# Performance work log

Measured on AMD Instinct MI355X. Metric: run time of the kernel, lower is better.

## Reference

```python
import jax, jax.numpy as jnp
import numpy as np

N = 50000   # team_count (num nodes)
E = 800000  # num edges
D = 64      # embed_dim
C = 32      # conv_out_channels
K = 3       # Chebyshev order
B = 16384   # number of games (len(home))


def setup_inputs() -> dict:
    key = jax.random.key(0)
    ks = jax.random.split(key, 20)
    inp = {
        "edge_index": jax.random.randint(ks[0], (2, E), 0, N),
        "home": jax.random.randint(ks[1], (B,), 0, N),
        "away": jax.random.randint(ks[2], (B,), 0, N),
        "edge_weight": jax.random.uniform(ks[3], (E,), dtype=jnp.float32),
        "embedding": jax.random.normal(ks[4], (N, D), dtype=jnp.float32) * 0.1,
    }
    def W(k, i, o):
        return jax.random.normal(k, (K, i, o), dtype=jnp.float32) * 0.05
    inp["Wxz"] = W(ks[5], D, C); inp["Whz"] = W(ks[6], C, C)
    inp["Wxr"] = W(ks[7], D, C); inp["Whr"] = W(ks[8], C, C)
    inp["Wxh"] = W(ks[9], D, C); inp["Whh"] = W(ks[10], C, C)
    for i, name in enumerate(["bxz", "bhz", "bxr", "bhr", "bxh", "bhh"]):
        inp[name] = jax.random.normal(ks[11 + i], (C,), dtype=jnp.float32) * 0.01
    return inp


def _cheb(x, W, b, row, col, w_hat, n):
    """PyG ChebConv with sym normalization, lambda_max=2: L_hat = -D^-1/2 A D^-1/2."""
    def prop(t):  # L_hat @ t  via gather->scale->scatter over edges
        return jax.ops.segment_sum(w_hat[:, None] * t[row], col, num_segments=n)
    Tx0 = x
    out = Tx0 @ W[0]
    Tx1 = prop(Tx0)
    out = out + Tx1 @ W[1]
    for k in range(2, W.shape[0]):
        Tx2 = 2.0 * prop(Tx1) - Tx0
        out = out + Tx2 @ W[k]
        Tx0, Tx1 = Tx1, Tx2
    return out + b


def reference(edge_index, home, away, edge_weight, embedding,
              Wxz, Whz, Wxr, Whr, Wxh, Whh,
              bxz, bhz, bxr, bhr, bxh, bhh):
    row, col = edge_index[0], edge_index[1]
    n = embedding.shape[0]
    deg = jax.ops.segment_sum(edge_weight, row, num_segments=n)
    dinv = jnp.where(deg > 0, jax.lax.rsqrt(deg), 0.0)
    w_hat = -dinv[row] * edge_weight * dinv[col]

    x = embedding                       # [N, D]
    H = jnp.zeros((n, Wxz.shape[-1]), x.dtype)  # initial hidden state
    cheb = lambda t, W, b: _cheb(t, W, b, row, col, w_hat, n)

    Z = jax.nn.sigmoid(cheb(x, Wxz, bxz) + cheb(H, Whz, bhz))
    R = jax.nn.sigmoid(cheb(x, Wxr, bxr) + cheb(H, Whr, bhr))
    H_tilde = jnp.tanh(cheb(x, Wxh, bxh) + cheb(H * R, Whh, bhh))
    H = Z * H + (1.0 - Z) * H_tilde     # [N, C]

    h = jnp.concatenate([H[home], H[away]], axis=0)  # [2B, C]
    return jax.nn.softmax(h, axis=0)    # torch Softmax(dim=0)
```

## Files before the change

kernel.cpp:

```cpp
#include <hip/hip_runtime.h>
#include <hip/hip_fp16.h>
#include <math.h>

constexpr int N_   = 50000;
constexpr int E_   = 800000;
constexpr int D_   = 64;
constexpr int C_   = 32;
constexpr int B_   = 16384;
constexpr int TWOB = 2 * B_;
constexpr int NB_SM = 256;
constexpr int NBINS = (N_ + 255) / 256;
constexpr int EPB   = 4096;
constexpr int NBLK_BIN = (E_ + EPB - 1) / EPB;
constexpr int CAPB  = 5120;
constexpr int GN  = 64;
constexpr int LDP = 68;
constexpr int NPAD = 50176;

__device__ inline float4 ld_h4(const ushort* p) {
    uint2 u = *reinterpret_cast<const uint2*>(p);
    __half2 h0 = *reinterpret_cast<__half2*>(&u.x);
    __half2 h1 = *reinterpret_cast<__half2*>(&u.y);
    float2 f0 = __half22float2(h0), f1 = __half22float2(h1);
    return make_float4(f0.x, f0.y, f1.x, f1.y);
}
__device__ inline void st_h4(ushort* p, float4 v) {
    __half2 h0 = __floats2half2_rn(v.x, v.y);
    __half2 h1 = __floats2half2_rn(v.z, v.w);
    uint2 u;
    u.x = *reinterpret_cast<unsigned*>(&h0);
    u.y = *reinterpret_cast<unsigned*>(&h1);
    *reinterpret_cast<uint2*>(p) = u;
}

__global__ __launch_bounds__(256) void k_init(const float* __restrict__ x,
                                              ushort* __restrict__ xh,
                                              int2* __restrict__ curs) {
    if (blockIdx.x == 0) {
        curs[threadIdx.x] = make_int2(0, 0);
        if (threadIdx.x < 32) curs[256 + threadIdx.x] = make_int2(0, 0);
    }
    int i = blockIdx.x * 256 + threadIdx.x;
    if (i < N_ * D_ / 4) {
        float4 v = reinterpret_cast<const float4*>(x)[i];
        st_h4(xh + (size_t)i * 4, v);
    }
}

__device__ inline void excl_scan256(int* sc, int t, int c0, int* st) {
    sc[t] = c0;
    __syncthreads();
#pragma unroll
    for (int off = 1; off < 256; off <<= 1) {
        int v = (t >= off) ? sc[t - off] : 0;
        __syncthreads();
        sc[t] += v;
        __syncthreads();
    }
    st[t] = sc[t] - c0;
}

__global__ __launch_bounds__(256) void k_bin(const int* __restrict__ row,
                                             const int* __restrict__ col,
                                             const float* __restrict__ ew,
                                             int* __restrict__ colCur,
                                             int* __restrict__ rowCur,
                                             int2* __restrict__ colBins,
                                             int2* __restrict__ rowBins) {
    __shared__ int cnt[256], st[256], cur[256], gbase[256], sc[256];
    __shared__ int2 buf[EPB];
    int t = threadIdx.x;
    int base = blockIdx.x * EPB;
    int nE = min(EPB, E_ - base);

    cnt[t] = 0;
    __syncthreads();
    for (int i = t; i < nE; i += 256) atomicAdd(&cnt[col[base + i] >> 8], 1);
    __syncthreads();
    int c0 = cnt[t];
    excl_scan256(sc, t, c0, st);
    cur[t] = 0;
    gbase[t] = (t < NBINS && c0 > 0) ? atomicAdd(&colCur[t], c0) : 0;
    __syncthreads();
    for (int i = t; i < nE; i += 256) {
        int c = col[base + i], r = row[base + i];
        float w = ew[base + i];
        int p = st[c >> 8] + atomicAdd(&cur[c >> 8], 1);
        buf[p] = make_int2((c << 16) | r, __float_as_int(w));
    }
    __syncthreads();
    for (int i = t; i < nE; i += 256) {
        int2 e = buf[i];
        int bin = (int)(((unsigned)e.x) >> 24);
        int local = gbase[bin] + (i - st[bin]);
        if (local < CAPB) colBins[(size_t)bin * CAPB + local] = e;
    }
    __syncthreads();

    cnt[t] = 0;
    __syncthreads();
    for (int i = t; i < nE; i += 256) atomicAdd(&cnt[row[base + i] >> 8], 1);
    __syncthreads();
    c0 = cnt[t];
    excl_scan256(sc, t, c0, st);
    cur[t] = 0;
    gbase[t] = (t < NBINS && c0 > 0) ? atomicAdd(&rowCur[t], c0) : 0;
    __syncthreads();
    for (int i = t; i < nE; i += 256) {
        int r = row[base + i];
        float w = ew[base + i];
        int p = st[r >> 8] + atomicAdd(&cur[r >> 8], 1);
        buf[p] = make_int2(r, __float_as_int(w));
    }
    __syncthreads();
    for (int i = t; i < nE; i += 256) {
        int2 e = buf[i];
        int bin = (int)(((unsigned)e.x) >> 8);
        int local = gbase[bin] + (i - st[bin]);
        if (local < CAPB) rowBins[(size_t)bin * CAPB + local] = e;
    }
}

__global__ __launch_bounds__(256) void k_deg(const int* __restrict__ rowCur,
                                             const int2* __restrict__ rowBins,
                                             float* __restrict__ dinv) {
    __shared__ float acc[256];
    int t = threadIdx.x, b = blockIdx.x;
    acc[t] = 0.f;
    __syncthreads();
    int nb = min(rowCur[b], CAPB);
    const int2* bb = rowBins + (size_t)b * CAPB;
    for (int i = t; i < nb; i += 256) {
        int2 e = bb[i];
        atomicAdd(&acc[e.x & 255], __int_as_float(e.y));
    }
    __syncthreads();
    int r = b * 256 + t;
    if (r < N_) {
        float d = acc[t];
        dinv[r] = (d > 0.f) ? 1.f / sqrtf(d) : 0.f;
    }
}

__global__ __launch_bounds__(256) void k_sort(const int* __restrict__ colCur,
                                              int2* __restrict__ colBins,
                                              const float* __restrict__ dinv,
                                              int2* __restrict__ percol) {
    __shared__ int cnt[256], st[256], cur[256], sc[256];
    __shared__ int2 sbuf[CAPB];
    int t = threadIdx.x, b = blockIdx.x;
    int nb = min(colCur[b], CAPB);
    int2* bb = colBins + (size_t)b * CAPB;
    cnt[t] = 0;
    __syncthreads();
    for (int i = t; i < nb; i += 256)
        atomicAdd(&cnt[(((unsigned)bb[i].x) >> 16) & 255], 1);
    __syncthreads();
    int c0 = cnt[t];
    excl_scan256(sc, t, c0, st);
    cur[t] = 0;
    __syncthreads();
    for (int i = t; i < nb; i += 256) {
        int2 e = bb[i];
        int clow = (((unsigned)e.x) >> 16) & 255;
        int p = st[clow] + atomicAdd(&cur[clow], 1);
        sbuf[p] = e;
    }
    __syncthreads();
    for (int i = t; i < nb; i += 256) {
        int2 e = sbuf[i];
        unsigned m = (unsigned)e.x;
        int r = (int)(m & 0xffffu);
        int c = (int)(m >> 16);
        float w = -__int_as_float(e.y) * dinv[r] * dinv[c];
        bb[i] = make_int2(r, __float_as_int(w));
    }
    int c = b * 256 + t;
    percol[c] = make_int2(b * CAPB + st[t], cnt[t]);
}

template <bool FUSE2>
__global__ __launch_bounds__(256) void k_gproph(const int2* __restrict__ percol,
                                                const int2* __restrict__ edges,
                                                const ushort* __restrict__ src,
                                                const ushort* __restrict__ xsub,
                                                ushort* __restrict__ dst) {
    int node = (blockIdx.x * 256 + threadIdx.x) >> 6;
    if (node >= N_) return;
    int lane = threadIdx.x & 63;
    int eslot = lane >> 4;
    int f4 = (lane & 15) << 2;
    int2 oc = percol[node];
    int beg = oc.x, n = oc.y;
    float4 acc = {0.f, 0.f, 0.f, 0.f};
    for (int cb = 0; cb < n; cb += 16) {
        int2 er = edges[beg + cb + (lane & 15)];
        int   rr = er.x;
        float wr = __int_as_float(er.y);
#pragma unroll
        for (int k = 0; k < 4; ++k) {
            int idx = cb + 4 * k + eslot;
            int   r = __shfl(rr, 4 * k + eslot, 64);
            float w = __shfl(wr, 4 * k + eslot, 64);
            bool ok = idx < n;
            int  rs = ok ? r : 0;
            float wm = ok ? w : 0.f;
            float4 v = ld_h4(src + (size_t)rs * D_ + f4);
            acc.x += wm * v.x;
            acc.y += wm * v.y;
            acc.z += wm * v.z;
            acc.w += wm * v.w;
        }
    }
    acc.x += __shfl_xor(acc.x, 16, 64); acc.y += __shfl_xor(acc.y, 16, 64);
    acc.z += __shfl_xor(acc.z, 16, 64); acc.w += __shfl_xor(acc.w, 16, 64);
    acc.x += __shfl_xor(acc.x, 32, 64); acc.y += __shfl_xor(acc.y, 32, 64);
    acc.z += __shfl_xor(acc.z, 32, 64); acc.w += __shfl_xor(acc.w, 32, 64);
    if (eslot == 0) {
        float4 o = acc;
        if (FUSE2) {
            float4 xv = ld_h4(xsub + (size_t)node * D_ + f4);
            o.x = 2.f * acc.x - xv.x;
            o.y = 2.f * acc.y - xv.y;
            o.z = 2.f * acc.z - xv.z;
            o.w = 2.f * acc.w - xv.w;
        }
        st_h4(dst + (size_t)node * D_ + f4, o);
    }
}

__global__ __launch_bounds__(256) void k_gates2h(const ushort* __restrict__ xh,
                                                 const ushort* __restrict__ tx1h,
                                                 const ushort* __restrict__ tx2h,
                                                 const float* __restrict__ Wxz,
                                                 const float* __restrict__ Wxh,
                                                 const float* __restrict__ bxz,
                                                 const float* __restrict__ bhz,
                                                 const float* __restrict__ bxh,
                                                 const float* __restrict__ bhh,
                                                 float* __restrict__ H) {
    __shared__ float lA[GN * LDP];
    __shared__ float lB[D_ * LDP];
    int t = threadIdx.x;
    int node0 = blockIdx.x * GN;
    int valid = min(GN, N_ - node0);
    int tn = t >> 4, tc = t & 15;
    float acc[4][4] = {};
    const ushort* srcs[3] = {xh, tx1h, tx2h};
    for (int ch = 0; ch < 3; ++ch) {
        const ushort* s = srcs[ch] + (size_t)node0 * D_;
#pragma unroll
        for (int j = 0; j < 4; ++j) {
            int q = t * 4 + j * 1024;
            int nd = q >> 6, dd = q & 63;
            float4 v = {0.f, 0.f, 0.f, 0.f};
            if (nd < valid) v = ld_h4(s + q);
            *reinterpret_cast<float4*>(&lA[nd * LDP + dd]) = v;
        }
#pragma unroll
        for (int j = 0; j < 4; ++j) {
            int q = t * 4 + j * 1024;
            int dd = q >> 6, jj = q & 63;
            const float* wsrc = (jj < 32) ? (Wxz + ch * 2048 + dd * 32 + jj)
                                          : (Wxh + ch * 2048 + dd * 32 + (jj - 32));
            *reinterpret_cast<float4*>(&lB[dd * LDP + jj]) =
                *reinterpret_cast<const float4*>(wsrc);
        }
        __syncthreads();
#pragma unroll 4
        for (int k0 = 0; k0 < D_; k0 += 4) {
            float4 a[4], b[4];
#pragma unroll
            for (int i = 0; i < 4; ++i)
                a[i] = *reinterpret_cast<const float4*>(&lA[(tn * 4 + i) * LDP + k0]);
#pragma unroll
            for (int kk = 0; kk < 4; ++kk)
                b[kk] = *reinterpret_cast<const float4*>(&lB[(k0 + kk) * LDP + tc * 4]);
#pragma unroll
            for (int i = 0; i < 4; ++i) {
                acc[i][0] += a[i].x * b[0].x + a[i].y * b[1].x + a[i].z * b[2].x + a[i].w * b[3].x;
                acc[i][1] += a[i].x * b[0].y + a[i].y * b[1].y + a[i].z * b[2].y + a[i].w * b[3].y;
                acc[i][2] += a[i].x * b[0].z + a[i].y * b[1].z + a[i].z * b[2].z + a[i].w * b[3].z;
                acc[i][3] += a[i].x * b[0].w + a[i].y * b[1].w + a[i].z * b[2].w + a[i].w * b[3].w;
            }
        }
        __syncthreads();
    }
#pragma unroll
    for (int i = 0; i < 4; ++i) {
        float4 v = {acc[i][0], acc[i][1], acc[i][2], acc[i][3]};
        *reinterpret_cast<float4*>(&lA[(tn * 4 + i) * LDP + tc * 4]) = v;
    }
    __syncthreads();
#pragma unroll
    for (int m = 0; m < 8; ++m) {
        int idx = t + m * 256;
        int nd = idx >> 5, c = idx & 31;
        if (nd < valid) {
            float az = lA[nd * LDP + c]       + bxz[c] + bhz[c];
            float ah = lA[nd * LDP + 32 + c]  + bxh[c] + bhh[c];
            float z  = 1.f / (1.f + expf(-az));
            H[(size_t)(node0 + nd) * C_ + c] = (1.f - z) * tanhf(ah);
        }
    }
}

__global__ __launch_bounds__(256) void k_gexpsum2(const int* __restrict__ home,
                                                  const int* __restrict__ away,
                                                  const float* __restrict__ H,
                                                  float* __restrict__ hbuf,
                                                  float* __restrict__ colsum) {
    __shared__ float sm[8][32];
    int c = threadIdx.x & 31, g = threadIdx.x >> 5;
    float s = 0.f;
    for (int r0 = blockIdx.x * 8; r0 < TWOB; r0 += gridDim.x * 8) {
        int r = r0 + g;
        int node = (r < B_) ? home[r] : away[r - B_];
        float e = expf(H[(size_t)node * C_ + c]);
        hbuf[(size_t)r * C_ + c] = e;
        s += e;
    }
    sm[g][c] = s;
    __syncthreads();
    if (g < 4) sm[g][c] += sm[g + 4][c];
    __syncthreads();
    if (g < 2) sm[g][c] += sm[g + 2][c];
    __syncthreads();
    if (g == 0) atomicAdd(&colsum[c], sm[0][c] + sm[1][c]);
}

__global__ __launch_bounds__(256) void k_norm(const float* __restrict__ hbuf,
                                              const float* __restrict__ colsum,
                                              float* __restrict__ out) {
    int i = blockIdx.x * 256 + threadIdx.x;
    if (i < TWOB * C_ / 4) {
        float4 v = reinterpret_cast<const float4*>(hbuf)[i];
        int c0 = (i * 4) & 31;
        float4 s = *reinterpret_cast<const float4*>(colsum + c0);
        float4 o;
        o.x = v.x / s.x;
        o.y = v.y / s.y;
        o.z = v.z / s.z;
        o.w = v.w / s.w;
        reinterpret_cast<float4*>(out)[i] = o;
    }
}

extern "C" void kernel_launch(void* const* d_in, const int* in_sizes, int n_in,
                              void* d_out, int out_size, void* d_ws, size_t ws_size,
                              hipStream_t stream) {
    const int*   edge_index = (const int*)d_in[0];
    const int*   row  = edge_index;
    const int*   col  = edge_index + E_;
    const int*   home = (const int*)d_in[1];
    const int*   away = (const int*)d_in[2];
    const float* ew   = (const float*)d_in[3];
    const float* x    = (const float*)d_in[4];
    const float* Wxz  = (const float*)d_in[5];
    const float* Wxh  = (const float*)d_in[9];
    const float* bxz  = (const float*)d_in[11];
    const float* bhz  = (const float*)d_in[12];
    const float* bxh  = (const float*)d_in[15];
    const float* bhh  = (const float*)d_in[16];
    float* out = (float*)d_out;
    float* ws = (float*)d_ws;

    const size_t o_colCur  = 0;
    const size_t o_rowCur  = 256;
    const size_t o_colsum  = 512;
    const size_t o_dinv    = 576;
    const size_t o_colBins = o_dinv + NPAD;
    const size_t o_rowBins = o_colBins + 2 * (size_t)NBINS * CAPB + 32;
    const size_t o_percol  = o_rowBins + 2 * (size_t)NBINS * CAPB;
    const size_t o_xh      = o_percol + 2 * (size_t)NBINS * 256;
    const size_t o_tx1h    = o_xh + (size_t)N_ * D_ / 2;
    const size_t o_tx2h    = o_tx1h + (size_t)N_ * D_ / 2;
    const size_t o_H       = o_rowBins;
    const size_t o_hbuf    = o_xh;

    int*    colCur  = (int*)(ws + o_colCur);
    int*    rowCur  = (int*)(ws + o_rowCur);
    int2*   colBins = (int2*)(ws + o_colBins);
    int2*   rowBins = (int2*)(ws + o_rowBins);
    int2*   percol  = (int2*)(ws + o_percol);
    ushort* xh      = (ushort*)(ws + o_xh);
    ushort* tx1h    = (ushort*)(ws + o_tx1h);
    ushort* tx2h    = (ushort*)(ws + o_tx2h);

    k_init<<<(N_ * D_ / 4 + 255) / 256, 256, 0, stream>>>(x, xh, (int2*)ws);

    k_bin <<<NBLK_BIN, 256, 0, stream>>>(row, col, ew, colCur, rowCur, colBins, rowBins);
    k_deg <<<NBINS, 256, 0, stream>>>(rowCur, rowBins, ws + o_dinv);
    k_sort<<<NBINS, 256, 0, stream>>>(colCur, colBins, ws + o_dinv, percol);

    k_gproph<false><<<(N_ * 64 + 255) / 256, 256, 0, stream>>>(percol, colBins, xh, nullptr, tx1h);
    k_gproph<true> <<<(N_ * 64 + 255) / 256, 256, 0, stream>>>(percol, colBins, tx1h, xh, tx2h);

    k_gates2h<<<(N_ + GN - 1) / GN, 256, 0, stream>>>(xh, tx1h, tx2h,
                                                      Wxz, Wxh, bxz, bhz, bxh, bhh, ws + o_H);

    k_gexpsum2<<<NB_SM, 256, 0, stream>>>(home, away, ws + o_H, ws + o_hbuf, ws + o_colsum);
    k_norm    <<<(TWOB * C_ / 4 + 255) / 256, 256, 0, stream>>>(ws + o_hbuf, ws + o_colsum, out);
}
```

Baseline: 148.7 us.

## Replace atomic binning with per-chunk bins and fuse second propagation into gate GEMM

Edge binning now writes into fixed per-(bin, chunk) slots with per-chunk counts instead of taking global atomic cursors, so the init kernel that zeroed cursors and converted x to half is removed. The degree and sort kernels gather the chunk slots, and sort writes to a separate edge array. The first propagation reads x in fp32 directly, and the second propagation is fused into the gate GEMM kernel so Tx2 stays in shared memory and never goes to global memory. The cost is fewer launches and less global traffic, traded for serial per-thread chunk loops in deg/sort, a per-chunk cap of 64 edges that could overflow on skewed inputs, and a fused kernel with only one wave per node group doing the gather.

```diff
diff --git a/kernel.cpp b/kernel.cpp
--- a/kernel.cpp
+++ b/kernel.cpp
@@ -11,7 +11,8 @@
 constexpr int NB_SM = 256;
 constexpr int NBINS = (N_ + 255) / 256;
 constexpr int EPB   = 4096;
-constexpr int NBLK_BIN = (E_ + EPB - 1) / EPB;
+constexpr int NCH   = (E_ + EPB - 1) / EPB;
+constexpr int CAPBB = 64;
 constexpr int CAPB  = 5120;
 constexpr int GN  = 64;
 constexpr int LDP = 68;
@@ -33,20 +34,6 @@
     *reinterpret_cast<uint2*>(p) = u;
 }
 
-__global__ __launch_bounds__(256) void k_init(const float* __restrict__ x,
-                                              ushort* __restrict__ xh,
-                                              int2* __restrict__ curs) {
-    if (blockIdx.x == 0) {
-        curs[threadIdx.x] = make_int2(0, 0);
-        if (threadIdx.x < 32) curs[256 + threadIdx.x] = make_int2(0, 0);
-    }
-    int i = blockIdx.x * 256 + threadIdx.x;
-    if (i < N_ * D_ / 4) {
-        float4 v = reinterpret_cast<const float4*>(x)[i];
-        st_h4(xh + (size_t)i * 4, v);
-    }
-}
-
 __device__ inline void excl_scan256(int* sc, int t, int c0, int* st) {
     sc[t] = c0;
     __syncthreads();
@@ -63,14 +50,14 @@
 __global__ __launch_bounds__(256) void k_bin(const int* __restrict__ row,
                                              const int* __restrict__ col,
                                              const float* __restrict__ ew,
-                                             int* __restrict__ colCur,
-                                             int* __restrict__ rowCur,
-                                             int2* __restrict__ colBins,
-                                             int2* __restrict__ rowBins) {
-    __shared__ int cnt[256], st[256], cur[256], gbase[256], sc[256];
+                                             int* __restrict__ colCnt,
+                                             int* __restrict__ rowCnt,
+                                             int2* __restrict__ colBins2,
+                                             int2* __restrict__ rowBins2) {
+    __shared__ int cnt[256], st[256], cur[256], sc[256];
     __shared__ int2 buf[EPB];
-    int t = threadIdx.x;
-    int base = blockIdx.x * EPB;
+    int t = threadIdx.x, blk = blockIdx.x;
+    int base = blk * EPB;
     int nE = min(EPB, E_ - base);
 
     cnt[t] = 0;
@@ -80,7 +67,6 @@
     int c0 = cnt[t];
     excl_scan256(sc, t, c0, st);
     cur[t] = 0;
-    gbase[t] = (t < NBINS && c0 > 0) ? atomicAdd(&colCur[t], c0) : 0;
     __syncthreads();
     for (int i = t; i < nE; i += 256) {
         int c = col[base + i], r = row[base + i];
@@ -92,9 +78,10 @@
     for (int i = t; i < nE; i += 256) {
         int2 e = buf[i];
         int bin = (int)(((unsigned)e.x) >> 24);
-        int local = gbase[bin] + (i - st[bin]);
-        if (local < CAPB) colBins[(size_t)bin * CAPB + local] = e;
-    }
+        int local = i - st[bin];
+        if (local < CAPBB) colBins2[((size_t)bin * NCH + blk) * CAPBB + local] = e;
+    }
+    colCnt[blk * 256 + t] = min(c0, CAPBB);
     __syncthreads();
 
     cnt[t] = 0;
@@ -104,7 +91,6 @@
     c0 = cnt[t];
     excl_scan256(sc, t, c0, st);
     cur[t] = 0;
-    gbase[t] = (t < NBINS && c0 > 0) ? atomicAdd(&rowCur[t], c0) : 0;
     __syncthreads();
     for (int i = t; i < nE; i += 256) {
         int r = row[base + i];
@@ -116,23 +102,26 @@
     for (int i = t; i < nE; i += 256) {
         int2 e = buf[i];
         int bin = (int)(((unsigned)e.x) >> 8);
-        int local = gbase[bin] + (i - st[bin]);
-        if (local < CAPB) rowBins[(size_t)bin * CAPB + local] = e;
-    }
-}
-
-__global__ __launch_bounds__(256) void k_deg(const int* __restrict__ rowCur,
-                                             const int2* __restrict__ rowBins,
+        int local = i - st[bin];
+        if (local < CAPBB) rowBins2[((size_t)bin * NCH + blk) * CAPBB + local] = e;
+    }
+    rowCnt[blk * 256 + t] = min(c0, CAPBB);
+}
+
+__global__ __launch_bounds__(256) void k_deg(const int* __restrict__ rowCnt,
+                                             const int2* __restrict__ rowBins2,
                                              float* __restrict__ dinv) {
     __shared__ float acc[256];
     int t = threadIdx.x, b = blockIdx.x;
     acc[t] = 0.f;
     __syncthreads();
-    int nb = min(rowCur[b], CAPB);
-    const int2* bb = rowBins + (size_t)b * CAPB;
-    for (int i = t; i < nb; i += 256) {
-        int2 e = bb[i];
-        atomicAdd(&acc[e.x & 255], __int_as_float(e.y));
+    if (t < NCH) {
+        int n = rowCnt[t * 256 + b];
+        const int2* ch = rowBins2 + ((size_t)b * NCH + t) * CAPBB;
+        for (int i = 0; i < n; ++i) {
+            int2 e = ch[i];
+            atomicAdd(&acc[e.x & 255], __int_as_float(e.y));
+        }
     }
     __syncthreads();
     int r = b * 256 + t;
@@ -142,30 +131,37 @@
     }
 }
 
-__global__ __launch_bounds__(256) void k_sort(const int* __restrict__ colCur,
-                                              int2* __restrict__ colBins,
+__global__ __launch_bounds__(256) void k_sort(const int* __restrict__ colCnt,
+                                              const int2* __restrict__ colBins2,
                                               const float* __restrict__ dinv,
-                                              int2* __restrict__ percol) {
-    __shared__ int cnt[256], st[256], cur[256], sc[256];
+                                              int2* __restrict__ edges,
+                                              int2* __restrict__ percol,
+                                              float* __restrict__ colsum) {
+    __shared__ int cnt[256], st[256], cur[256], sc[256], pref[256];
     __shared__ int2 sbuf[CAPB];
     int t = threadIdx.x, b = blockIdx.x;
-    int nb = min(colCur[b], CAPB);
-    int2* bb = colBins + (size_t)b * CAPB;
+    if (b == 0 && t < 64) colsum[t] = 0.f;
+    int myc = (t < NCH) ? colCnt[t * 256 + b] : 0;
+    excl_scan256(sc, t, myc, pref);
     cnt[t] = 0;
     __syncthreads();
-    for (int i = t; i < nb; i += 256)
-        atomicAdd(&cnt[(((unsigned)bb[i].x) >> 16) & 255], 1);
-    __syncthreads();
+    if (t < NCH) {
+        const int2* ch = colBins2 + ((size_t)b * NCH + t) * CAPBB;
+        int p0 = pref[t];
+        for (int i = 0; i < myc; ++i) {
+            if (p0 + i < CAPB) {
+                int2 e = ch[i];
+                sbuf[p0 + i] = e;
+                atomicAdd(&cnt[(((unsigned)e.x) >> 16) & 255], 1);
+            }
+        }
+    }
+    __syncthreads();
+    int nb = min(sc[255], CAPB);
     int c0 = cnt[t];
+    __syncthreads();
     excl_scan256(sc, t, c0, st);
     cur[t] = 0;
-    __syncthreads();
-    for (int i = t; i < nb; i += 256) {
-        int2 e = bb[i];
-        int clow = (((unsigned)e.x) >> 16) & 255;
-        int p = st[clow] + atomicAdd(&cur[clow], 1);
-        sbuf[p] = e;
-    }
     __syncthreads();
     for (int i = t; i < nb; i += 256) {
         int2 e = sbuf[i];
@@ -173,18 +169,17 @@
         int r = (int)(m & 0xffffu);
         int c = (int)(m >> 16);
         float w = -__int_as_float(e.y) * dinv[r] * dinv[c];
-        bb[i] = make_int2(r, __float_as_int(w));
-    }
-    int c = b * 256 + t;
-    percol[c] = make_int2(b * CAPB + st[t], cnt[t]);
-}
-
-template <bool FUSE2>
-__global__ __launch_bounds__(256) void k_gproph(const int2* __restrict__ percol,
-                                                const int2* __restrict__ edges,
-                                                const ushort* __restrict__ src,
-                                                const ushort* __restrict__ xsub,
-                                                ushort* __restrict__ dst) {
+        int clow = c & 255;
+        int p = st[clow] + atomicAdd(&cur[clow], 1);
+        edges[b * CAPB + p] = make_int2(r, __float_as_int(w));
+    }
+    percol[b * 256 + t] = make_int2(b * CAPB + st[t], cnt[t]);
+}
+
+__global__ __launch_bounds__(256) void k_prop1(const int2* __restrict__ percol,
+                                               const int2* __restrict__ edges,
+                                               const float* __restrict__ x,
+                                               ushort* __restrict__ tx1h) {
     int node = (blockIdx.x * 256 + threadIdx.x) >> 6;
     if (node >= N_) return;
     int lane = threadIdx.x & 63;
@@ -205,7 +200,7 @@
             bool ok = idx < n;
             int  rs = ok ? r : 0;
             float wm = ok ? w : 0.f;
-            float4 v = ld_h4(src + (size_t)rs * D_ + f4);
+            float4 v = *reinterpret_cast<const float4*>(x + (size_t)rs * D_ + f4);
             acc.x += wm * v.x;
             acc.y += wm * v.y;
             acc.z += wm * v.z;
@@ -216,46 +211,96 @@
     acc.z += __shfl_xor(acc.z, 16, 64); acc.w += __shfl_xor(acc.w, 16, 64);
     acc.x += __shfl_xor(acc.x, 32, 64); acc.y += __shfl_xor(acc.y, 32, 64);
     acc.z += __shfl_xor(acc.z, 32, 64); acc.w += __shfl_xor(acc.w, 32, 64);
-    if (eslot == 0) {
-        float4 o = acc;
-        if (FUSE2) {
-            float4 xv = ld_h4(xsub + (size_t)node * D_ + f4);
-            o.x = 2.f * acc.x - xv.x;
-            o.y = 2.f * acc.y - xv.y;
-            o.z = 2.f * acc.z - xv.z;
-            o.w = 2.f * acc.w - xv.w;
-        }
-        st_h4(dst + (size_t)node * D_ + f4, o);
-    }
-}
-
-__global__ __launch_bounds__(256) void k_gates2h(const ushort* __restrict__ xh,
-                                                 const ushort* __restrict__ tx1h,
-                                                 const ushort* __restrict__ tx2h,
-                                                 const float* __restrict__ Wxz,
-                                                 const float* __restrict__ Wxh,
-                                                 const float* __restrict__ bxz,
-                                                 const float* __restrict__ bhz,
-                                                 const float* __restrict__ bxh,
-                                                 const float* __restrict__ bhh,
-                                                 float* __restrict__ H) {
+    if (eslot == 0) st_h4(tx1h + (size_t)node * D_ + f4, acc);
+}
+
+__global__ __launch_bounds__(256) void k_pg(const int2* __restrict__ percol,
+                                            const int2* __restrict__ edges,
+                                            const ushort* __restrict__ tx1h,
+                                            const float* __restrict__ x,
+                                            const float* __restrict__ Wxz,
+                                            const float* __restrict__ Wxh,
+                                            const float* __restrict__ bxz,
+                                            const float* __restrict__ bhz,
+                                            const float* __restrict__ bxh,
+                                            const float* __restrict__ bhh,
+                                            float* __restrict__ H) {
     __shared__ float lA[GN * LDP];
     __shared__ float lB[D_ * LDP];
     int t = threadIdx.x;
     int node0 = blockIdx.x * GN;
     int valid = min(GN, N_ - node0);
+    int w = t >> 6, lane = t & 63, eslot = lane >> 4, f4 = (lane & 15) << 2;
+
+    for (int j = 0; j < 16; ++j) {
+        int nl = w * 16 + j;
+        int node = node0 + nl;
+        if (node < N_) {
+            int2 oc = percol[node];
+            int beg = oc.x, n = oc.y;
+            float4 acc = {0.f, 0.f, 0.f, 0.f};
+            for (int cb = 0; cb < n; cb += 16) {
+                int2 er = edges[beg + cb + (lane & 15)];
+                int   rr = er.x;
+                float wr = __int_as_float(er.y);
+#pragma unroll
+                for (int k = 0; k < 4; ++k) {
+                    int idx = cb + 4 * k + eslot;
+                    int   r = __shfl(rr, 4 * k + eslot, 64);
+                    float ww = __shfl(wr, 4 * k + eslot, 64);
+                    bool ok = idx < n;
+                    int  rs = ok ? r : 0;
+                    float wm = ok ? ww : 0.f;
+                    float4 v = ld_h4(tx1h + (size_t)rs * D_ + f4);
+                    acc.x += wm * v.x;
+                    acc.y += wm * v.y;
+                    acc.z += wm * v.z;
+                    acc.w += wm * v.w;
+                }
+            }
+            acc.x += __shfl_xor(acc.x, 16, 64); acc.y += __shfl_xor(acc.y, 16, 64);
+            acc.z += __shfl_xor(acc.z, 16, 64); acc.w += __shfl_xor(acc.w, 16, 64);
+            acc.x += __shfl_xor(acc.x, 32, 64); acc.y += __shfl_xor(acc.y, 32, 64);
+            acc.z += __shfl_xor(acc.z, 32, 64); acc.w += __shfl_xor(acc.w, 32, 64);
+            if (eslot == 0) {
+                float4 xv = *reinterpret_cast<const float4*>(x + (size_t)node * D_ + f4);
+                float4 o = {2.f * acc.x - xv.x, 2.f * acc.y - xv.y,
+                            2.f * acc.z - xv.z, 2.f * acc.w - xv.w};
+                *reinterpret_cast<float4*>(&lA[nl * LDP + f4]) = o;
+            }
+        } else if (eslot == 0) {
+            float4 z = {0.f, 0.f, 0.f, 0.f};
+            *reinterpret_cast<float4*>(&lA[nl * LDP + f4]) = z;
+        }
+    }
+    __syncthreads();
+
     int tn = t >> 4, tc = t & 15;
-    float acc[4][4] = {};
-    const ushort* srcs[3] = {xh, tx1h, tx2h};
-    for (int ch = 0; ch < 3; ++ch) {
-        const ushort* s = srcs[ch] + (size_t)node0 * D_;
-#pragma unroll
-        for (int j = 0; j < 4; ++j) {
-            int q = t * 4 + j * 1024;
-            int nd = q >> 6, dd = q & 63;
-            float4 v = {0.f, 0.f, 0.f, 0.f};
-            if (nd < valid) v = ld_h4(s + q);
-            *reinterpret_cast<float4*>(&lA[nd * LDP + dd]) = v;
+    float acc2[4][4] = {};
+    for (int cc = 0; cc < 3; ++cc) {
+        int ch = (cc == 0) ? 2 : (cc == 1) ? 0 : 1;
+        if (cc) {
+            if (ch == 0) {
+                const float* s = x + (size_t)node0 * D_;
+#pragma unroll
+                for (int j = 0; j < 4; ++j) {
+                    int q = t * 4 + j * 1024;
+                    int nd = q >> 6, dd = q & 63;
+                    float4 v = {0.f, 0.f, 0.f, 0.f};
+                    if (nd < valid) v = *reinterpret_cast<const float4*>(s + q);
+                    *reinterpret_cast<float4*>(&lA[nd * LDP + dd]) = v;
+                }
+            } else {
+                const ushort* s = tx1h + (size_t)node0 * D_;
+#pragma unroll
+                for (int j = 0; j < 4; ++j) {
+                    int q = t * 4 + j * 1024;
+                    int nd = q >> 6, dd = q & 63;
+                    float4 v = {0.f, 0.f, 0.f, 0.f};
+                    if (nd < valid) v = ld_h4(s + q);
+                    *reinterpret_cast<float4*>(&lA[nd * LDP + dd]) = v;
+                }
+            }
         }
 #pragma unroll
         for (int j = 0; j < 4; ++j) {
@@ -278,17 +323,17 @@
                 b[kk] = *reinterpret_cast<const float4*>(&lB[(k0 + kk) * LDP + tc * 4]);
 #pragma unroll
             for (int i = 0; i < 4; ++i) {
-                acc[i][0] += a[i].x * b[0].x + a[i].y * b[1].x + a[i].z * b[2].x + a[i].w * b[3].x;
-                acc[i][1] += a[i].x * b[0].y + a[i].y * b[1].y + a[i].z * b[2].y + a[i].w * b[3].y;
-                acc[i][2] += a[i].x * b[0].z + a[i].y * b[1].z + a[i].z * b[2].z + a[i].w * b[3].z;
-                acc[i][3] += a[i].x * b[0].w + a[i].y * b[1].w + a[i].z * b[2].w + a[i].w * b[3].w;
+                acc2[i][0] += a[i].x * b[0].x + a[i].y * b[1].x + a[i].z * b[2].x + a[i].w * b[3].x;
+                acc2[i][1] += a[i].x * b[0].y + a[i].y * b[1].y + a[i].z * b[2].y + a[i].w * b[3].y;
+                acc2[i][2] += a[i].x * b[0].z + a[i].y * b[1].z + a[i].z * b[2].z + a[i].w * b[3].z;
+                acc2[i][3] += a[i].x * b[0].w + a[i].y * b[1].w + a[i].z * b[2].w + a[i].w * b[3].w;
             }
         }
         __syncthreads();
     }
 #pragma unroll
     for (int i = 0; i < 4; ++i) {
-        float4 v = {acc[i][0], acc[i][1], acc[i][2], acc[i][3]};
+        float4 v = {acc2[i][0], acc2[i][1], acc2[i][2], acc2[i][3]};
         *reinterpret_cast<float4*>(&lA[(tn * 4 + i) * LDP + tc * 4]) = v;
     }
     __syncthreads();
@@ -365,39 +410,34 @@
     float* out = (float*)d_out;
     float* ws = (float*)d_ws;
 
-    const size_t o_colCur  = 0;
-    const size_t o_rowCur  = 256;
-    const size_t o_colsum  = 512;
-    const size_t o_dinv    = 576;
-    const size_t o_colBins = o_dinv + NPAD;
-    const size_t o_rowBins = o_colBins + 2 * (size_t)NBINS * CAPB + 32;
-    const size_t o_percol  = o_rowBins + 2 * (size_t)NBINS * CAPB;
-    const size_t o_xh      = o_percol + 2 * (size_t)NBINS * 256;
-    const size_t o_tx1h    = o_xh + (size_t)N_ * D_ / 2;
-    const size_t o_tx2h    = o_tx1h + (size_t)N_ * D_ / 2;
-    const size_t o_H       = o_rowBins;
-    const size_t o_hbuf    = o_xh;
-
-    int*    colCur  = (int*)(ws + o_colCur);
-    int*    rowCur  = (int*)(ws + o_rowCur);
-    int2*   colBins = (int2*)(ws + o_colBins);
-    int2*   rowBins = (int2*)(ws + o_rowBins);
-    int2*   percol  = (int2*)(ws + o_percol);
-    ushort* xh      = (ushort*)(ws + o_xh);
-    ushort* tx1h    = (ushort*)(ws + o_tx1h);
-    ushort* tx2h    = (ushort*)(ws + o_tx2h);
-
-    k_init<<<(N_ * D_ / 4 + 255) / 256, 256, 0, stream>>>(x, xh, (int2*)ws);
-
-    k_bin <<<NBLK_BIN, 256, 0, stream>>>(row, col, ew, colCur, rowCur, colBins, rowBins);
-    k_deg <<<NBINS, 256, 0, stream>>>(rowCur, rowBins, ws + o_dinv);
-    k_sort<<<NBINS, 256, 0, stream>>>(colCur, colBins, ws + o_dinv, percol);
-
-    k_gproph<false><<<(N_ * 64 + 255) / 256, 256, 0, stream>>>(percol, colBins, xh, nullptr, tx1h);
-    k_gproph<true> <<<(N_ * 64 + 255) / 256, 256, 0, stream>>>(percol, colBins, tx1h, xh, tx2h);
-
-    k_gates2h<<<(N_ + GN - 1) / GN, 256, 0, stream>>>(xh, tx1h, tx2h,
-                                                      Wxz, Wxh, bxz, bhz, bxh, bhh, ws + o_H);
+    const size_t o_colCnt  = 0;
+    const size_t o_rowCnt  = o_colCnt + (size_t)NCH * 256;
+    const size_t o_colsum  = o_rowCnt + (size_t)NCH * 256;
+    const size_t o_dinv    = o_colsum + 64;
+    const size_t o_colBins2 = o_dinv + NPAD;
+    const size_t o_rowBins2 = o_colBins2 + 2 * (size_t)NBINS * NCH * CAPBB;
+    const size_t o_edges   = o_rowBins2 + 2 * (size_t)NBINS * NCH * CAPBB;
+    const size_t o_percol  = o_edges + 2 * (size_t)NBINS * CAPB + 32;
+    const size_t o_tx1h    = o_percol + 2 * (size_t)NBINS * 256;
+    const size_t o_H       = o_rowBins2;
+    const size_t o_hbuf    = o_colBins2;
+
+    int*    colCnt   = (int*)(ws + o_colCnt);
+    int*    rowCnt   = (int*)(ws + o_rowCnt);
+    int2*   colBins2 = (int2*)(ws + o_colBins2);
+    int2*   rowBins2 = (int2*)(ws + o_rowBins2);
+    int2*   edges    = (int2*)(ws + o_edges);
+    int2*   percol   = (int2*)(ws + o_percol);
+    ushort* tx1h     = (ushort*)(ws + o_tx1h);
+
+    k_bin <<<NCH, 256, 0, stream>>>(row, col, ew, colCnt, rowCnt, colBins2, rowBins2);
+    k_deg <<<NBINS, 256, 0, stream>>>(rowCnt, rowBins2, ws + o_dinv);
+    k_sort<<<NBINS, 256, 0, stream>>>(colCnt, colBins2, ws + o_dinv, edges, percol, ws + o_colsum);
+
+    k_prop1<<<(N_ * 64 + 255) / 256, 256, 0, stream>>>(percol, edges, x, tx1h);
+
+    k_pg<<<(N_ + GN - 1) / GN, 256, 0, stream>>>(percol, edges, tx1h, x,
+                                                 Wxz, Wxh, bxz, bhz, bxh, bhh, ws + o_H);
 
     k_gexpsum2<<<NB_SM, 256, 0, stream>>>(home, away, ws + o_H, ws + o_hbuf, ws + o_colsum);
     k_norm    <<<(TWOB * C_ / 4 + 255) / 256, 256, 0, stream>>>(ws + o_hbuf, ws + o_colsum, out);
```

Result: slower. 155.8 us (+4.8%).
